# Kernel optimization log

Hardware: AMD Instinct MI355X
Metric: run time of the kernel (lower is better)

Reference implementation:

```python
import jax, jax.numpy as jnp
from jax import lax
import numpy as np

NUM_HEADS = 8
KW = 3  # window kernel size

def _avgpool3(x):
    # x: [B,C,H,W]; AvgPool2d(3,1,1) with count_include_pad=True -> sum/9
    s = lax.reduce_window(x, 0.0, lax.add, (1, 1, KW, KW), (1, 1, 1, 1),
                          ((0, 0), (0, 0), (1, 1), (1, 1)))
    return s / (KW * KW)

def _unfold3(y):
    # y: [B,h,w,C] -> [B,h,w,9,C]; patch index ordered row-major (kh,kw)
    B, h, w, C = y.shape
    yp = jnp.pad(y, ((0, 0), (1, 1), (1, 1), (0, 0)))
    return jnp.stack([yp[:, i:i + h, j:j + w, :]
                      for i in range(KW) for j in range(KW)], axis=3)

def setup_inputs():
    key = jax.random.key(0)
    ks = jax.random.split(key, 9)
    B, C, H, W = 8, 256, 64, 64
    sd = 0.02
    return {
        "x": jax.random.normal(ks[0], (B, C, H, W), jnp.float32),
        "W_qkv": jax.random.normal(ks[1], (4 * C, C), jnp.float32) * sd,
        "b_qkv": jnp.zeros((4 * C,), jnp.float32),
        "W1": jax.random.normal(ks[2], (C // 2, C), jnp.float32) * sd,
        "b1": jnp.zeros((C // 2,), jnp.float32),
        "W2": jax.random.normal(ks[3], (C, C // 2), jnp.float32) * sd,
        "b2": jnp.zeros((C,), jnp.float32),
        "Wp": jax.random.normal(ks[4], (C, C), jnp.float32) * sd,
        "bp": jnp.zeros((C,), jnp.float32),
    }

def reference(x, W_qkv, b_qkv, W1, b1, W2, b2, Wp, bp):
    B, C, H, W = x.shape
    nH = NUM_HEADS
    hd = C // nH
    scale = hd ** -0.5
    # avg pool (stride 1 keeps spatial dims), to channels-last
    y = _avgpool3(x).transpose(0, 2, 3, 1)                 # [B,h,w,C]
    qkv = y @ W_qkv.T + b_qkv                              # [B,h,w,4C]
    qkv = qkv.reshape(B, H, W, C, 4)
    q, k, v, chans = qkv[..., 0], qkv[..., 1], qkv[..., 2], qkv[..., 3]
    # channel gate
    g = jax.nn.sigmoid(jax.nn.relu(chans @ W1.T + b1) @ W2.T + b2)  # [B,h,w,C]
    # local window attention: each query attends to its 3x3 neighborhood
    qh = q.reshape(B, H, W, nH, hd)                        # [B,h,w,n,d]
    kp = _unfold3(k).reshape(B, H, W, KW * KW, nH, hd)     # [B,h,w,9,n,d]
    vp = _unfold3(v).reshape(B, H, W, KW * KW, nH, hd)
    attn = jnp.einsum('bhwnd,bhwknd->bhwnk', qh, kp) * scale
    attn = jax.nn.softmax(attn, axis=-1)
    out = jnp.einsum('bhwnk,bhwknd->bhwnd', attn, vp).reshape(B, H, W, C)
    out = out * g + out
    out = out @ Wp.T + bp
    return out.transpose(0, 3, 1, 2)                       # [B,C,H,W]
```

## Files before the change

kernel.cpp:

```cpp
#include <hip/hip_runtime.h>
#include <stdint.h>

typedef __bf16    bf16x8 __attribute__((ext_vector_type(8)));
typedef float     f32x4  __attribute__((ext_vector_type(4)));
typedef uint32_t  u32x4  __attribute__((ext_vector_type(4)));
typedef uint32_t  u32x2  __attribute__((ext_vector_type(2)));

#define MFMA(a,b,c) __builtin_amdgcn_mfma_f32_16x16x32_bf16((a),(b),(c),0,0,0)

__device__ __align__(16) uint16_t g_y [8*64*64*256];
__device__ __align__(16) uint16_t g_wpk[393216];

#define WQF 0
#define WKF 65536
#define WVF 131072
#define WCF 196608
#define W1F 262144
#define W2F 294912
#define WPF 327680

static __device__ __forceinline__ float b2f(uint32_t u){ return __builtin_bit_cast(float, u<<16); }
static __device__ __forceinline__ float blo(uint32_t u){ return __builtin_bit_cast(float, u<<16); }
static __device__ __forceinline__ float bhi(uint32_t u){ return __builtin_bit_cast(float, u & 0xffff0000u); }
static __device__ __forceinline__ uint16_t f2bn(float f){
  return __builtin_bit_cast(uint16_t, (__bf16)f);
}
static __device__ __forceinline__ uint32_t pk2(float x, float y){
  return (uint32_t)f2bn(x) | ((uint32_t)f2bn(y) << 16);
}

__global__ __launch_bounds__(512) void kprep(const float* __restrict__ x,
    const float* __restrict__ Wqkv, const float* __restrict__ W1,
    const float* __restrict__ W2, const float* __restrict__ Wp){
  int t = threadIdx.x;
  int bid = blockIdx.x;
  if (bid < 512){
    __shared__ __align__(16) uint16_t sm[10*32*82];
    uint32_t* smw = (uint32_t*)sm;
    int b = bid >> 6, rem = bid & 63;
    int hg = rem >> 3, cg = rem & 7;
    int h0 = hg*8, ch = cg*32;
    for (int i=t; i<320; i+=512){
      int base = i*41;
      smw[base+3]  = 0;
      smw[base+36] = 0;
    }
    if (hg==0){
      for (int i=t; i<1312; i+=512) smw[i] = 0;
    }
    if (hg==7){
      for (int i=t; i<1312; i+=512) smw[9*1312 + i] = 0;
    }
    #pragma unroll
    for (int i=0;i<10;i++){
      int id = t + 512*i;
      int w4 = id&15, c = (id>>4)&31, hh = id>>9;
      int gy = h0 - 1 + hh;
      if ((unsigned)gy < 64u){
        f32x4 ld = *(const f32x4*)&x[(((b*256+ch+c)*64+gy)*64) + w4*4];
        int wb = (((hh*32+c)*82 + 8 + w4*4) >> 1);
        smw[wb+0] = pk2(ld[0], ld[1]);
        smw[wb+1] = pk2(ld[2], ld[3]);
      }
    }
    __syncthreads();
    int c = t & 31, wsel = (t >> 5) & 1, py = t >> 6;
    int r0 = ((py+0)*32+c)*82, r1 = ((py+1)*32+c)*82, r2 = ((py+2)*32+c)*82;
    int w0 = wsel*32;
    float csp = b2f(sm[r0+w0+7]) + b2f(sm[r1+w0+7]) + b2f(sm[r2+w0+7]);
    float csc = b2f(sm[r0+w0+8]) + b2f(sm[r1+w0+8]) + b2f(sm[r2+w0+8]);
    uint16_t* dst = g_y + ((b*64 + h0 + py)*64)*256 + ch + c;
    for (int j2=0;j2<32;j2++){
      int w = w0 + j2;
      float csn = b2f(sm[r0+w+9]) + b2f(sm[r1+w+9]) + b2f(sm[r2+w+9]);
      float yv = (csp + csc + csn) * (1.0f/9.0f);
      dst[w*256] = f2bn(yv);
      csp = csc; csc = csn;
    }
  } else {
    int idx = (bid - 512)*512 + t;
    int j = idx & 7, lane = (idx>>3)&63;
    int n16 = lane & 15, q4 = lane>>4;
    float v;
    if (idx < 262144){
      int tt = idx >> 16, l = idx & 65535;
      int s = (l>>9)&7, nt = l>>12;
      v = Wqkv[(4*(nt*16+n16) + tt)*256 + s*32 + q4*8 + j];
    } else if (idx < 294912){
      int l = idx - 262144;
      int s = (l>>9)&7, nt = l>>12;
      v = W1[(nt*16+n16)*256 + s*32 + q4*8 + j];
    } else if (idx < 327680){
      int l = idx - 294912;
      int s = (l>>9)&3, nt = l>>11;
      v = W2[(nt*16+n16)*128 + s*32 + q4*8 + j];
    } else {
      int l = idx - 327680;
      int s = (l>>9)&7, nt = l>>12;
      v = Wp[(nt*16+n16)*256 + s*32 + q4*8 + j];
    }
    g_wpk[idx] = f2bn(v);
  }
}

#define YSTR  264
#define HSTR  136
#define K2_QS 15840
#define K2_KS 20192
#define K2_VS 28352
#define MCH   0
#define MHS   8448
#define MAO   15840
#define MAOSTR 266
#define MAOT  15840
#define MTSTR 36
__global__ __launch_bounds__(512,4) void kattn(const float* __restrict__ bqkv,
    const float* __restrict__ b1, const float* __restrict__ b2v,
    const float* __restrict__ bp, float* __restrict__ out){
  __shared__ __align__(16) uint16_t sm[36512];
  int t = threadIdx.x;
  int lane = t & 63, wave = t >> 6;
  int n16 = lane & 15, quad = lane >> 4;
  int bid = blockIdx.x;
  int bb = bid >> 7, ty = (bid >> 3) & 15, tx = bid & 7;

  uint32_t opk[2][8];
  uint32_t chp[16];

  int hrow0 = 10*(n16>>3) + (n16&7) + 11;
  int hrow1 = hrow0 + 20;

  #pragma unroll
  for (int i=0;i<4;i++){
    int id = t + 512*i;
    if (id < 1920){
      int hp = id >> 5, c8 = id & 31;
      int py = hp/10, px = hp - py*10;
      int gy = ty*4 + py - 1, gx = tx*8 + px - 1;
      u32x4 ld = {0,0,0,0};
      if ((unsigned)gy<64u && (unsigned)gx<64u)
        ld = *(const u32x4*)&g_y[((bb*64+gy)*64+gx)*256 + c8*8];
      *(u32x4*)&sm[hp*YSTR + c8*8] = ld;
    }
  }
  __syncthreads();

  #pragma unroll
  for (int hf=0; hf<2; hf++){
    {
      int ntg = hf*8 + wave;
      bf16x8 Bq[8];
      #pragma unroll
      for (int s=0;s<8;s++) Bq[s] = *(const bf16x8*)&g_wpk[WQF + ((ntg*8+s)*64+lane)*8];
      float bq = bqkv[4*(ntg*16+n16) + 0];
      int colB = wave*16;
      #pragma unroll
      for (int mt=0; mt<2; mt++){
        f32x4 a = {0.f,0.f,0.f,0.f};
        int hrow = mt ? hrow1 : hrow0;
        #pragma unroll
        for (int s=0;s<8;s++){
          bf16x8 A = *(const bf16x8*)&sm[hrow*YSTR + s*32 + quad*8];
          a = MFMA(A, Bq[s], a);
        }
        #pragma unroll
        for (int r=0;r<4;r++){
          int row = mt*16 + quad*4 + r;
          sm[K2_QS + row*HSTR + colB + n16] = f2bn(a[r] + bq);
        }
      }
    }
    {
      int ntg = hf*8 + wave;
      bf16x8 Bk[8], Bv[8];
      #pragma unroll
      for (int s=0;s<8;s++){
        Bk[s] = *(const bf16x8*)&g_wpk[WKF + ((ntg*8+s)*64+lane)*8];
        Bv[s] = *(const bf16x8*)&g_wpk[WVF + ((ntg*8+s)*64+lane)*8];
      }
      float bk = bqkv[4*(ntg*16+n16) + 1];
      float bv = bqkv[4*(ntg*16+n16) + 2];
      int colB = wave*16;
      #pragma unroll
      for (int mt=0; mt<4; mt++){
        f32x4 ak = {0.f,0.f,0.f,0.f}, av = {0.f,0.f,0.f,0.f};
        int m = mt*16 + n16;
        int mr = (m < 60) ? m : 59;
        #pragma unroll
        for (int s=0;s<8;s++){
          bf16x8 A = *(const bf16x8*)&sm[mr*YSTR + s*32 + quad*8];
          ak = MFMA(A, Bk[s], ak);
          av = MFMA(A, Bv[s], av);
        }
        #pragma unroll
        for (int r=0;r<4;r++){
          int row = mt*16 + quad*4 + r;
          if (row < 60){
            int py = row/10, px = row - py*10;
            int gy = ty*4 + py - 1, gx = tx*8 + px - 1;
            bool ok = ((unsigned)gy<64u) && ((unsigned)gx<64u);
            sm[K2_KS + row*HSTR + colB + n16] = ok ? f2bn(ak[r] + bk) : (uint16_t)0;
            sm[K2_VS + row*HSTR + colB + n16] = ok ? f2bn(av[r] + bv) : (uint16_t)0;
          }
        }
      }
    }
    __syncthreads();
    if (wave < 4){
      int p = lane & 31, half = lane >> 5;
      int cb = wave*32 + half*16;
      const uint16_t* qp = &sm[K2_QS + p*HSTR + cb];
      u32x4 qa = *(const u32x4*)qp;
      u32x4 qb = *(const u32x4*)(qp+8);
      float qv[16];
      #pragma unroll
      for (int i=0;i<4;i++){
        qv[2*i]    = blo(qa[i]); qv[2*i+1]   = bhi(qa[i]);
        qv[8+2*i]  = blo(qb[i]); qv[8+2*i+1] = bhi(qb[i]);
      }
      int hb = 10*(p>>3) + (p&7) + 11;
      const int off[9] = {-11,-10,-9,-1,0,1,9,10,11};
      float sc[9];
      #pragma unroll
      for (int nb=0;nb<9;nb++){
        const uint16_t* kp = &sm[K2_KS + (hb+off[nb])*HSTR + cb];
        u32x4 ka = *(const u32x4*)kp;
        u32x4 kb = *(const u32x4*)(kp+8);
        float s = 0.f;
        #pragma unroll
        for (int i=0;i<4;i++){
          s += qv[2*i]*blo(ka[i])   + qv[2*i+1]*bhi(ka[i]);
          s += qv[8+2*i]*blo(kb[i]) + qv[8+2*i+1]*bhi(kb[i]);
        }
        s += __shfl_xor(s, 32);
        sc[nb] = s * 0.17677669529663687f;
      }
      float mx = sc[0];
      #pragma unroll
      for (int nb=1;nb<9;nb++) mx = fmaxf(mx, sc[nb]);
      float l = 0.f;
      #pragma unroll
      for (int nb=0;nb<9;nb++){ sc[nb] = __expf(sc[nb]-mx); l += sc[nb]; }
      float inv = 1.f / l;
      float o[16];
      #pragma unroll
      for (int i=0;i<16;i++) o[i]=0.f;
      #pragma unroll
      for (int nb=0;nb<9;nb++){
        float wgt = sc[nb]*inv;
        const uint16_t* vp = &sm[K2_VS + (hb+off[nb])*HSTR + cb];
        u32x4 va = *(const u32x4*)vp;
        u32x4 vb = *(const u32x4*)(vp+8);
        #pragma unroll
        for (int i=0;i<4;i++){
          o[2*i]    += wgt*blo(va[i]); o[2*i+1]   += wgt*bhi(va[i]);
          o[8+2*i]  += wgt*blo(vb[i]); o[8+2*i+1] += wgt*bhi(vb[i]);
        }
      }
      #pragma unroll
      for (int i=0;i<8;i++) opk[hf][i] = pk2(o[2*i], o[2*i+1]);
    } else if (hf == 0){
      f32x4 cc[4][2];
      #pragma unroll
      for (int jj=0;jj<4;jj++){
        cc[jj][0] = f32x4{0.f,0.f,0.f,0.f};
        cc[jj][1] = f32x4{0.f,0.f,0.f,0.f};
      }
      #pragma unroll
      for (int s=0;s<8;s++){
        bf16x8 A0 = *(const bf16x8*)&sm[hrow0*YSTR + s*32 + quad*8];
        bf16x8 A1 = *(const bf16x8*)&sm[hrow1*YSTR + s*32 + quad*8];
        #pragma unroll
        for (int jj=0;jj<4;jj++){
          int ntg = (wave-4)*4 + jj;
          bf16x8 Bc = *(const bf16x8*)&g_wpk[WCF + ((ntg*8+s)*64+lane)*8];
          cc[jj][0] = MFMA(A0, Bc, cc[jj][0]);
          cc[jj][1] = MFMA(A1, Bc, cc[jj][1]);
        }
      }
      #pragma unroll
      for (int jj=0;jj<4;jj++){
        int ntg = (wave-4)*4 + jj;
        float bc = bqkv[4*(ntg*16+n16) + 3];
        #pragma unroll
        for (int mt=0;mt<2;mt++){
          chp[(jj*2+mt)*2+0] = pk2(cc[jj][mt][0]+bc, cc[jj][mt][1]+bc);
          chp[(jj*2+mt)*2+1] = pk2(cc[jj][mt][2]+bc, cc[jj][mt][3]+bc);
        }
      }
    } else {
      #pragma unroll
      for (int jj=0;jj<4;jj++){
        int ntg = (wave-4)*4 + jj;
        int col = ntg*16 + n16;
        #pragma unroll
        for (int mt=0;mt<2;mt++){
          #pragma unroll
          for (int r2=0;r2<2;r2++){
            uint32_t v = chp[(jj*2+mt)*2+r2];
            int row = mt*16 + quad*4 + r2*2;
            sm[MCH + row*264 + col]     = (uint16_t)(v & 0xffffu);
            sm[MCH + (row+1)*264 + col] = (uint16_t)(v >> 16);
          }
        }
      }
    }
    __syncthreads();
  }
  if (wave < 4){
    int p = lane & 31, half = lane >> 5;
    int cb = wave*32 + half*16;
    #pragma unroll
    for (int hf=0;hf<2;hf++)
      #pragma unroll
      for (int i=0;i<8;i++)
        *(uint32_t*)&sm[MAO + p*MAOSTR + hf*128 + cb + 2*i] = opk[hf][i];
  }
  {
    int ntg = wave;
    bf16x8 Bf[8];
    #pragma unroll
    for (int s=0;s<8;s++) Bf[s] = *(const bf16x8*)&g_wpk[W1F + ((ntg*8+s)*64+lane)*8];
    float bs = b1[ntg*16+n16];
    int colB = wave*16;
    #pragma unroll
    for (int mt=0;mt<2;mt++){
      f32x4 a = {0.f,0.f,0.f,0.f};
      #pragma unroll
      for (int s=0;s<8;s++){
        bf16x8 A = *(const bf16x8*)&sm[MCH + (mt*16+n16)*264 + s*32 + quad*8];
        a = MFMA(A, Bf[s], a);
      }
      #pragma unroll
      for (int r=0;r<4;r++){
        int row = mt*16 + quad*4 + r;
        sm[MHS + row*HSTR + colB + n16] = f2bn(fmaxf(a[r]+bs, 0.f));
      }
    }
  }
  __syncthreads();
  {
    int nt0 = wave*2, nt1 = nt0+1;
    f32x4 g00={0.f,0.f,0.f,0.f}, g01={0.f,0.f,0.f,0.f};
    f32x4 g10={0.f,0.f,0.f,0.f}, g11={0.f,0.f,0.f,0.f};
    #pragma unroll
    for (int s=0;s<4;s++){
      bf16x8 B0 = *(const bf16x8*)&g_wpk[W2F + ((nt0*4+s)*64+lane)*8];
      bf16x8 B1 = *(const bf16x8*)&g_wpk[W2F + ((nt1*4+s)*64+lane)*8];
      bf16x8 A0 = *(const bf16x8*)&sm[MHS + n16*HSTR + s*32 + quad*8];
      bf16x8 A1 = *(const bf16x8*)&sm[MHS + (16+n16)*HSTR + s*32 + quad*8];
      g00 = MFMA(A0,B0,g00); g01 = MFMA(A1,B0,g01);
      g10 = MFMA(A0,B1,g10); g11 = MFMA(A1,B1,g11);
    }
    float bs0 = b2v[nt0*16+n16], bs1 = b2v[nt1*16+n16];
    #pragma unroll
    for (int jj=0;jj<2;jj++){
      int colB = (wave*2+jj)*16;
      float bs = jj ? bs1 : bs0;
      #pragma unroll
      for (int mt=0;mt<2;mt++){
        f32x4 a = jj ? (mt ? g11 : g10) : (mt ? g01 : g00);
        #pragma unroll
        for (int r=0;r<4;r++){
          int row = mt*16 + quad*4 + r;
          float gg = 1.f/(1.f+__expf(-(a[r] + bs)));
          float ao = b2f((uint32_t)sm[MAO + row*MAOSTR + colB + n16]);
          sm[MCH + row*264 + colB + n16] = f2bn(ao*(1.f+gg));
        }
      }
    }
  }
  __syncthreads();
  {
    int nt0 = wave*2, nt1 = nt0+1;
    f32x4 p00={0.f,0.f,0.f,0.f}, p01={0.f,0.f,0.f,0.f};
    f32x4 p10={0.f,0.f,0.f,0.f}, p11={0.f,0.f,0.f,0.f};
    #pragma unroll
    for (int s=0;s<8;s++){
      bf16x8 B0 = *(const bf16x8*)&g_wpk[WPF + ((nt0*8+s)*64+lane)*8];
      bf16x8 B1 = *(const bf16x8*)&g_wpk[WPF + ((nt1*8+s)*64+lane)*8];
      bf16x8 A0 = *(const bf16x8*)&sm[MCH + n16*264 + s*32 + quad*8];
      bf16x8 A1 = *(const bf16x8*)&sm[MCH + (16+n16)*264 + s*32 + quad*8];
      p00 = MFMA(A0,B0,p00); p01 = MFMA(A1,B0,p01);
      p10 = MFMA(A0,B1,p10); p11 = MFMA(A1,B1,p11);
    }
    float bs0 = bp[nt0*16+n16], bs1 = bp[nt1*16+n16];
    #pragma unroll
    for (int jj=0;jj<2;jj++){
      int col = (wave*2+jj)*16 + n16;
      float bs = jj ? bs1 : bs0;
      #pragma unroll
      for (int mt=0;mt<2;mt++){
        f32x4 a = jj ? (mt ? p11 : p10) : (mt ? p01 : p00);
        u32x2 pk = { pk2(a[0]+bs, a[1]+bs), pk2(a[2]+bs, a[3]+bs) };
        int row0 = mt*16 + quad*4;
        *(u32x2*)&sm[MAOT + col*MTSTR + row0] = pk;
      }
    }
  }
  __syncthreads();
  #pragma unroll
  for (int i=0;i<4;i++){
    int idx = t + 512*i;
    int ix4 = idx&1, iy = (idx>>1)&3, c = idx>>3;
    int p0 = iy*8 + ix4*4;
    u32x2 pk = *(const u32x2*)&sm[MAOT + c*MTSTR + p0];
    f32x4 stv;
    stv[0] = blo(pk[0]); stv[1] = bhi(pk[0]);
    stv[2] = blo(pk[1]); stv[3] = bhi(pk[1]);
    *(f32x4*)&out[(((bb*256+c)*64) + ty*4+iy)*64 + tx*8 + ix4*4] = stv;
  }
}

extern "C" void kernel_launch(void* const* d_in, const int* in_sizes, int n_in,
                              void* d_out, int out_size, void* d_ws, size_t ws_size,
                              hipStream_t stream){
  (void)in_sizes; (void)n_in; (void)d_ws; (void)ws_size; (void)out_size;
  const float* x    = (const float*)d_in[0];
  const float* Wqkv = (const float*)d_in[1];
  const float* bqkv = (const float*)d_in[2];
  const float* W1   = (const float*)d_in[3];
  const float* b1   = (const float*)d_in[4];
  const float* W2   = (const float*)d_in[5];
  const float* b2   = (const float*)d_in[6];
  const float* Wp   = (const float*)d_in[7];
  const float* bp   = (const float*)d_in[8];
  kprep<<<dim3(1280), dim3(512), 0, stream>>>(x, Wqkv, W1, W2, Wp);
  kattn<<<dim3(1024), dim3(512), 0, stream>>>(bqkv, b1, b2, bp, (float*)d_out);
}
```

Baseline: 175.5 us.

## Spread second-half window attention across all eight waves

In the second channel-half iteration, the window attention now runs on all 8 waves instead of only 4. Each lane handles 8 channels of a head and reduces the dot products with an extra cross-lane shuffle. Waves 4-7 previously only stored the channel-gate results to shared memory in that phase, so they were mostly idle. The change is meant to balance work across waves and shorten the critical path, at the cost of an extra shuffle per score and a different output register layout.

```diff
diff --git a/kernel.cpp b/kernel.cpp
--- a/kernel.cpp
+++ b/kernel.cpp
@@ -124,7 +124,8 @@
   int bid = blockIdx.x;
   int bb = bid >> 7, ty = (bid >> 3) & 15, tx = bid & 7;
 
-  uint32_t opk[2][8];
+  uint32_t opk0[8];
+  uint32_t opk1[4];
   uint32_t chp[16];
 
   int hrow0 = 10*(n16>>3) + (n16&7) + 11;
@@ -206,18 +207,99 @@
       }
     }
     __syncthreads();
-    if (wave < 4){
-      int p = lane & 31, half = lane >> 5;
-      int cb = wave*32 + half*16;
+    if (hf == 0){
+      if (wave < 4){
+        int p = lane & 31, half = lane >> 5;
+        int cb = wave*32 + half*16;
+        const uint16_t* qp = &sm[K2_QS + p*HSTR + cb];
+        u32x4 qa = *(const u32x4*)qp;
+        u32x4 qb = *(const u32x4*)(qp+8);
+        float qv[16];
+        #pragma unroll
+        for (int i=0;i<4;i++){
+          qv[2*i]    = blo(qa[i]); qv[2*i+1]   = bhi(qa[i]);
+          qv[8+2*i]  = blo(qb[i]); qv[8+2*i+1] = bhi(qb[i]);
+        }
+        int hb = 10*(p>>3) + (p&7) + 11;
+        const int off[9] = {-11,-10,-9,-1,0,1,9,10,11};
+        float sc[9];
+        #pragma unroll
+        for (int nb=0;nb<9;nb++){
+          const uint16_t* kp = &sm[K2_KS + (hb+off[nb])*HSTR + cb];
+          u32x4 ka = *(const u32x4*)kp;
+          u32x4 kb = *(const u32x4*)(kp+8);
+          float s = 0.f;
+          #pragma unroll
+          for (int i=0;i<4;i++){
+            s += qv[2*i]*blo(ka[i])   + qv[2*i+1]*bhi(ka[i]);
+            s += qv[8+2*i]*blo(kb[i]) + qv[8+2*i+1]*bhi(kb[i]);
+          }
+          s += __shfl_xor(s, 32);
+          sc[nb] = s * 0.17677669529663687f;
+        }
+        float mx = sc[0];
+        #pragma unroll
+        for (int nb=1;nb<9;nb++) mx = fmaxf(mx, sc[nb]);
+        float l = 0.f;
+        #pragma unroll
+        for (int nb=0;nb<9;nb++){ sc[nb] = __expf(sc[nb]-mx); l += sc[nb]; }
+        float inv = 1.f / l;
+        float o[16];
+        #pragma unroll
+        for (int i=0;i<16;i++) o[i]=0.f;
+        #pragma unroll
+        for (int nb=0;nb<9;nb++){
+          float wgt = sc[nb]*inv;
+          const uint16_t* vp = &sm[K2_VS + (hb+off[nb])*HSTR + cb];
+          u32x4 va = *(const u32x4*)vp;
+          u32x4 vb = *(const u32x4*)(vp+8);
+          #pragma unroll
+          for (int i=0;i<4;i++){
+            o[2*i]    += wgt*blo(va[i]); o[2*i+1]   += wgt*bhi(va[i]);
+            o[8+2*i]  += wgt*blo(vb[i]); o[8+2*i+1] += wgt*bhi(vb[i]);
+          }
+        }
+        #pragma unroll
+        for (int i=0;i<8;i++) opk0[i] = pk2(o[2*i], o[2*i+1]);
+      } else {
+        f32x4 cc[4][2];
+        #pragma unroll
+        for (int jj=0;jj<4;jj++){
+          cc[jj][0] = f32x4{0.f,0.f,0.f,0.f};
+          cc[jj][1] = f32x4{0.f,0.f,0.f,0.f};
+        }
+        #pragma unroll
+        for (int s=0;s<8;s++){
+          bf16x8 A0 = *(const bf16x8*)&sm[hrow0*YSTR + s*32 + quad*8];
+          bf16x8 A1 = *(const bf16x8*)&sm[hrow1*YSTR + s*32 + quad*8];
+          #pragma unroll
+          for (int jj=0;jj<4;jj++){
+            int ntg = (wave-4)*4 + jj;
+            bf16x8 Bc = *(const bf16x8*)&g_wpk[WCF + ((ntg*8+s)*64+lane)*8];
+            cc[jj][0] = MFMA(A0, Bc, cc[jj][0]);
+            cc[jj][1] = MFMA(A1, Bc, cc[jj][1]);
+          }
+        }
+        #pragma unroll
+        for (int jj=0;jj<4;jj++){
+          int ntg = (wave-4)*4 + jj;
+          float bc = bqkv[4*(ntg*16+n16) + 3];
+          #pragma unroll
+          for (int mt=0;mt<2;mt++){
+            chp[(jj*2+mt)*2+0] = pk2(cc[jj][mt][0]+bc, cc[jj][mt][1]+bc);
+            chp[(jj*2+mt)*2+1] = pk2(cc[jj][mt][2]+bc, cc[jj][mt][3]+bc);
+          }
+        }
+      }
+    } else {
+      int head = wave >> 1, phalf = wave & 1, part = lane >> 4;
+      int p = phalf*16 + (lane & 15);
+      int cb = head*32 + part*8;
       const uint16_t* qp = &sm[K2_QS + p*HSTR + cb];
       u32x4 qa = *(const u32x4*)qp;
-      u32x4 qb = *(const u32x4*)(qp+8);
-      float qv[16];
-      #pragma unroll
-      for (int i=0;i<4;i++){
-        qv[2*i]    = blo(qa[i]); qv[2*i+1]   = bhi(qa[i]);
-        qv[8+2*i]  = blo(qb[i]); qv[8+2*i+1] = bhi(qb[i]);
-      }
+      float qv[8];
+      #pragma unroll
+      for (int i=0;i<4;i++){ qv[2*i]=blo(qa[i]); qv[2*i+1]=bhi(qa[i]); }
       int hb = 10*(p>>3) + (p&7) + 11;
       const int off[9] = {-11,-10,-9,-1,0,1,9,10,11};
       float sc[9];
@@ -225,13 +307,11 @@
       for (int nb=0;nb<9;nb++){
         const uint16_t* kp = &sm[K2_KS + (hb+off[nb])*HSTR + cb];
         u32x4 ka = *(const u32x4*)kp;
-        u32x4 kb = *(const u32x4*)(kp+8);
         float s = 0.f;
         #pragma unroll
-        for (int i=0;i<4;i++){
-          s += qv[2*i]*blo(ka[i])   + qv[2*i+1]*bhi(ka[i]);
-          s += qv[8+2*i]*blo(kb[i]) + qv[8+2*i+1]*bhi(kb[i]);
-        }
+        for (int i=0;i<4;i++)
+          s += qv[2*i]*blo(ka[i]) + qv[2*i+1]*bhi(ka[i]);
+        s += __shfl_xor(s, 16);
         s += __shfl_xor(s, 32);
         sc[nb] = s * 0.17677669529663687f;
       }
@@ -242,65 +322,35 @@
       #pragma unroll
       for (int nb=0;nb<9;nb++){ sc[nb] = __expf(sc[nb]-mx); l += sc[nb]; }
       float inv = 1.f / l;
-      float o[16];
-      #pragma unroll
-      for (int i=0;i<16;i++) o[i]=0.f;
+      float o[8];
+      #pragma unroll
+      for (int i=0;i<8;i++) o[i]=0.f;
       #pragma unroll
       for (int nb=0;nb<9;nb++){
         float wgt = sc[nb]*inv;
         const uint16_t* vp = &sm[K2_VS + (hb+off[nb])*HSTR + cb];
         u32x4 va = *(const u32x4*)vp;
-        u32x4 vb = *(const u32x4*)(vp+8);
         #pragma unroll
         for (int i=0;i<4;i++){
-          o[2*i]    += wgt*blo(va[i]); o[2*i+1]   += wgt*bhi(va[i]);
-          o[8+2*i]  += wgt*blo(vb[i]); o[8+2*i+1] += wgt*bhi(vb[i]);
-        }
-      }
-      #pragma unroll
-      for (int i=0;i<8;i++) opk[hf][i] = pk2(o[2*i], o[2*i+1]);
-    } else if (hf == 0){
-      f32x4 cc[4][2];
-      #pragma unroll
-      for (int jj=0;jj<4;jj++){
-        cc[jj][0] = f32x4{0.f,0.f,0.f,0.f};
-        cc[jj][1] = f32x4{0.f,0.f,0.f,0.f};
-      }
-      #pragma unroll
-      for (int s=0;s<8;s++){
-        bf16x8 A0 = *(const bf16x8*)&sm[hrow0*YSTR + s*32 + quad*8];
-        bf16x8 A1 = *(const bf16x8*)&sm[hrow1*YSTR + s*32 + quad*8];
+          o[2*i] += wgt*blo(va[i]); o[2*i+1] += wgt*bhi(va[i]);
+        }
+      }
+      #pragma unroll
+      for (int i=0;i<4;i++) opk1[i] = pk2(o[2*i], o[2*i+1]);
+      if (wave >= 4){
         #pragma unroll
         for (int jj=0;jj<4;jj++){
           int ntg = (wave-4)*4 + jj;
-          bf16x8 Bc = *(const bf16x8*)&g_wpk[WCF + ((ntg*8+s)*64+lane)*8];
-          cc[jj][0] = MFMA(A0, Bc, cc[jj][0]);
-          cc[jj][1] = MFMA(A1, Bc, cc[jj][1]);
-        }
-      }
-      #pragma unroll
-      for (int jj=0;jj<4;jj++){
-        int ntg = (wave-4)*4 + jj;
-        float bc = bqkv[4*(ntg*16+n16) + 3];
-        #pragma unroll
-        for (int mt=0;mt<2;mt++){
-          chp[(jj*2+mt)*2+0] = pk2(cc[jj][mt][0]+bc, cc[jj][mt][1]+bc);
-          chp[(jj*2+mt)*2+1] = pk2(cc[jj][mt][2]+bc, cc[jj][mt][3]+bc);
-        }
-      }
-    } else {
-      #pragma unroll
-      for (int jj=0;jj<4;jj++){
-        int ntg = (wave-4)*4 + jj;
-        int col = ntg*16 + n16;
-        #pragma unroll
-        for (int mt=0;mt<2;mt++){
+          int col = ntg*16 + n16;
           #pragma unroll
-          for (int r2=0;r2<2;r2++){
-            uint32_t v = chp[(jj*2+mt)*2+r2];
-            int row = mt*16 + quad*4 + r2*2;
-            sm[MCH + row*264 + col]     = (uint16_t)(v & 0xffffu);
-            sm[MCH + (row+1)*264 + col] = (uint16_t)(v >> 16);
+          for (int mt=0;mt<2;mt++){
+            #pragma unroll
+            for (int r2=0;r2<2;r2++){
+              uint32_t v = chp[(jj*2+mt)*2+r2];
+              int row = mt*16 + quad*4 + r2*2;
+              sm[MCH + row*264 + col]     = (uint16_t)(v & 0xffffu);
+              sm[MCH + (row+1)*264 + col] = (uint16_t)(v >> 16);
+            }
           }
         }
       }
@@ -311,10 +361,16 @@
     int p = lane & 31, half = lane >> 5;
     int cb = wave*32 + half*16;
     #pragma unroll
-    for (int hf=0;hf<2;hf++)
-      #pragma unroll
-      for (int i=0;i<8;i++)
-        *(uint32_t*)&sm[MAO + p*MAOSTR + hf*128 + cb + 2*i] = opk[hf][i];
+    for (int i=0;i<8;i++)
+      *(uint32_t*)&sm[MAO + p*MAOSTR + cb + 2*i] = opk0[i];
+  }
+  {
+    int head = wave >> 1, phalf = wave & 1, part = lane >> 4;
+    int p = phalf*16 + (lane & 15);
+    int cb = 128 + head*32 + part*8;
+    #pragma unroll
+    for (int i=0;i<4;i++)
+      *(uint32_t*)&sm[MAO + p*MAOSTR + cb + 2*i] = opk1[i];
   }
   {
     int ntg = wave;
```

Result: slower. 179.4 us (+2.2%).
